# Optimization experiments

Measured on AMD Instinct MI355X. Metric: run time of the kernel, lower is better.

Reference implementation:

```python
import jax, jax.numpy as jnp
import numpy as np

NEG_SLOPE = 0.2

def _gat_conv(x, src, dst, W, a_src, a_dst, b, heads, out_ch, concat):
    N = x.shape[0]
    h = (x @ W).reshape(N, heads, out_ch)                      # [N,H,C]
    al_s = jnp.einsum('nhc,hc->nh', h, a_src)                  # [N,H]
    al_d = jnp.einsum('nhc,hc->nh', h, a_dst)
    e = jax.nn.leaky_relu(al_s[src] + al_d[dst], NEG_SLOPE)    # [E,H]
    emax = jax.ops.segment_max(e, dst, num_segments=N)         # [N,H]
    ex = jnp.exp(e - emax[dst])
    denom = jax.ops.segment_sum(ex, dst, num_segments=N)
    alpha = ex / denom[dst]                                    # [E,H]
    msg = h[src] * alpha[:, :, None]                           # [E,H,C]
    out = jax.ops.segment_sum(msg, dst, num_segments=N)        # [N,H,C]
    if concat:
        out = out.reshape(N, heads * out_ch)
    else:
        out = out.mean(axis=1)
    return out + b

def _add_self_loops(edge_index, N):
    loops = jnp.arange(N, dtype=edge_index.dtype)
    src = jnp.concatenate([edge_index[0], loops])
    dst = jnp.concatenate([edge_index[1], loops])
    return src, dst

def setup_inputs() -> dict:
    key = jax.random.key(0)
    ks = jax.random.split(key, 16)
    N, E, Fin, C, H, G, OUT = 50000, 1600000, 128, 32, 8, 256, 64
    s = 0.05
    inp = {
        'x': jax.random.normal(ks[0], (N, Fin), jnp.float32),
        'edge_index': jax.random.randint(ks[1], (2, E), 0, N, jnp.int64),
        'batch': jnp.sort(jax.random.randint(ks[2], (N,), 0, G, jnp.int64)),
        'W0': jax.random.normal(ks[3], (Fin, H * C), jnp.float32) * s,
        'a_src0': jax.random.normal(ks[4], (H, C), jnp.float32) * s,
        'a_dst0': jax.random.normal(ks[5], (H, C), jnp.float32) * s,
        'b0': jnp.zeros((H * C,), jnp.float32),
        'W1': jax.random.normal(ks[6], (H * C, H * C), jnp.float32) * s,
        'a_src1': jax.random.normal(ks[7], (H, C), jnp.float32) * s,
        'a_dst1': jax.random.normal(ks[8], (H, C), jnp.float32) * s,
        'b1': jnp.zeros((H * C,), jnp.float32),
        'W2': jax.random.normal(ks[9], (H * C, C), jnp.float32) * s,
        'a_src2': jax.random.normal(ks[10], (1, C), jnp.float32) * s,
        'a_dst2': jax.random.normal(ks[11], (1, C), jnp.float32) * s,
        'b2': jnp.zeros((C,), jnp.float32),
        'lin_w': jax.random.normal(ks[12], (C, OUT), jnp.float32) * s,
        'lin_b': jnp.zeros((OUT,), jnp.float32),
    }
    return inp

def reference(x, edge_index, batch, W0, a_src0, a_dst0, b0, W1, a_src1, a_dst1, b1,
              W2, a_src2, a_dst2, b2, lin_w, lin_b):
    N = x.shape[0]
    G = 256
    src, dst = _add_self_loops(edge_index, N)
    h = jax.nn.relu(_gat_conv(x, src, dst, W0, a_src0, a_dst0, b0, 8, 32, True))
    h = jax.nn.relu(_gat_conv(h, src, dst, W1, a_src1, a_dst1, b1, 8, 32, True))
    h = _gat_conv(h, src, dst, W2, a_src2, a_dst2, b2, 1, 32, True)  # heads=1 concat -> [N,32]
    # global mean pool over graphs
    sums = jax.ops.segment_sum(h, batch, num_segments=G)
    cnts = jax.ops.segment_sum(jnp.ones((N,), h.dtype), batch, num_segments=G)
    pooled = sums / jnp.maximum(cnts, 1.0)[:, None]
    return pooled @ lin_w + lin_b
```

## Files before the change

### kernel.cpp

```cpp
#include <hip/hip_runtime.h>
#include <hip/hip_bf16.h>


#define LRELU(x) ((x) >= 0.f ? (x) : 0.2f * (x))

typedef unsigned short ushort8 __attribute__((ext_vector_type(8)));
typedef unsigned short ushort4v __attribute__((ext_vector_type(4)));
typedef __attribute__((ext_vector_type(8))) short bf16x8;
typedef __attribute__((ext_vector_type(4))) float f32x4;
typedef __attribute__((ext_vector_type(2))) float f32x2;

__device__ __forceinline__ float bf2f(unsigned short u) {
    return __uint_as_float(((unsigned)u) << 16);
}
__device__ __forceinline__ unsigned short f2bf(float f) {
    __hip_bfloat16 b = __float2bfloat16(f);
    return *reinterpret_cast<unsigned short*>(&b);
}
__device__ __forceinline__ void gl_lds16(const unsigned short* g, unsigned short* l) {
    __builtin_amdgcn_global_load_lds((const __attribute__((address_space(1))) void*)g,
                                     (__attribute__((address_space(3))) void*)l, 16, 0, 0);
}


__global__ void deg_kernel(const int* __restrict__ dst, int* __restrict__ deg,
                           int E, int N) {
    int i = blockIdx.x * blockDim.x + threadIdx.x;
    if (i < E) atomicAdd(&deg[dst[i]], 1);
    else if (i < E + N) atomicAdd(&deg[i - E], 1);
}

__global__ void scan_kernel(const int* __restrict__ deg, int* __restrict__ rowptr,
                            int n) {
    __shared__ int partial[1024];
    const int tid = threadIdx.x;
    const int chunk = (n + 1023) / 1024;
    const int start = min(tid * chunk, n);
    const int end = min(start + chunk, n);
    int s = 0;
    for (int i = start; i < end; i++) s += deg[i];
    partial[tid] = s;
    __syncthreads();
    for (int o = 1; o < 1024; o <<= 1) {
        int v = (tid >= o) ? partial[tid - o] : 0;
        __syncthreads();
        partial[tid] += v;
        __syncthreads();
    }
    int run = (tid == 0) ? 0 : partial[tid - 1];
    for (int i = start; i < end; i++) { rowptr[i] = run; run += deg[i]; }
    if (tid == 0) rowptr[n] = partial[1023];
}

__global__ void scatter_col_binned(const int* __restrict__ src, const int* __restrict__ dst,
                                   int* __restrict__ rowptr, int* __restrict__ col,
                                   int E, int N, int lo, int hi) {
    int i = blockIdx.x * blockDim.x + threadIdx.x;
    if (i < E) {
        int d = dst[i];
        if (d < lo || d >= hi) return;
        int pos = atomicAdd(&rowptr[d], 1);
        col[pos] = src[i];
    } else if (i < E + N) {
        int d = i - E;
        if (d < lo || d >= hi) return;
        int pos = atomicAdd(&rowptr[d], 1);
        col[pos] = d;
    }
}

__global__ void expand_dst_kernel(const int* __restrict__ rowptr, int* __restrict__ dstA,
                                  int N) {
    int n = blockIdx.x * blockDim.x + threadIdx.x;
    if (n >= N) return;
    int r0 = (n == 0) ? 0 : rowptr[n - 1];
    int r1 = rowptr[n];
    for (int p = r0; p < r1; p++) dstA[p] = n;
}

__global__ void gstart_kernel(const int* __restrict__ batch, int* __restrict__ gstart,
                              int N, int G) {
    int g = blockIdx.x * blockDim.x + threadIdx.x;
    if (g > G) return;
    int lo = 0, hi = N;
    while (lo < hi) { int mid = (lo + hi) >> 1; if (batch[mid] < g) lo = mid + 1; else hi = mid; }
    gstart[g] = lo;
}


__global__ void split_plain_kernel(const float* __restrict__ X, unsigned short* __restrict__ h,
                                   unsigned short* __restrict__ l, int n) {
    int i = blockIdx.x * blockDim.x + threadIdx.x;
    if (i >= n) return;
    float v = X[i];
    unsigned short hb = f2bf(v);
    h[i] = hb;
    l[i] = f2bf(v - bf2f(hb));
}

__global__ void splitT_kernel(const float* __restrict__ W, unsigned short* __restrict__ th,
                              unsigned short* __restrict__ tl, int K, int N) {
    int i = blockIdx.x * blockDim.x + threadIdx.x;
    if (i >= N * K) return;
    int n = i / K, k = i - n * K;
    float v = W[(size_t)k * N + n];
    unsigned short hb = f2bf(v);
    th[i] = hb;
    tl[i] = f2bf(v - bf2f(hb));
}


template <int BM, int BN, int WM, int WN>
__global__ __launch_bounds__(256)
void gemm_mfma_v2(const unsigned short* __restrict__ Ah, const unsigned short* __restrict__ Al,
                  const unsigned short* __restrict__ Bth, const unsigned short* __restrict__ Btl,
                  unsigned short* __restrict__ Cc, int M, int N, int K) {
    constexpr int BK = 32;
    constexpr int MT = WM / 16, NT = WN / 16;
    constexpr int NWX = BN / WN;
    __shared__ __attribute__((aligned(16))) unsigned short Ha[BM][BK];
    __shared__ __attribute__((aligned(16))) unsigned short La[BM][BK];
    __shared__ __attribute__((aligned(16))) unsigned short Hb[BN][BK];
    __shared__ __attribute__((aligned(16))) unsigned short Lb[BN][BK];
    const int tid = threadIdx.x;
    const int lane = tid & 63;
    const int wave = tid >> 6;
    const int wx = wave % NWX, wy = wave / NWX;
    const int by = blockIdx.y * BM;
    const int bx = blockIdx.x * BN;
    const int r16 = lane & 15, kg = lane >> 4;
    const int srow = lane >> 2, sslot = lane & 3;

    f32x4 acc[MT][NT];
#pragma unroll
    for (int i = 0; i < MT; i++)
#pragma unroll
        for (int j = 0; j < NT; j++) acc[i][j] = (f32x4){0.f, 0.f, 0.f, 0.f};

    for (int k0 = 0; k0 < K; k0 += BK) {
        for (int t = wave; t < BM / 16; t += 4) {
            int gm = by + t * 16 + srow;
            if (gm >= M) gm = M - 1;
            const size_t goff = (size_t)gm * K + k0 + sslot * 8;
            gl_lds16(Ah + goff, &Ha[t * 16][0]);
            gl_lds16(Al + goff, &La[t * 16][0]);
        }
        for (int t = wave; t < BN / 16; t += 4) {
            int gn = bx + t * 16 + srow;
            const size_t goff = (size_t)gn * K + k0 + sslot * 8;
            gl_lds16(Bth + goff, &Hb[t * 16][0]);
            gl_lds16(Btl + goff, &Lb[t * 16][0]);
        }
        __syncthreads();
        bf16x8 bh[NT], bl[NT];
#pragma unroll
        for (int j = 0; j < NT; j++) {
            bh[j] = *(const bf16x8*)&Hb[wx * WN + j * 16 + r16][kg * 8];
            bl[j] = *(const bf16x8*)&Lb[wx * WN + j * 16 + r16][kg * 8];
        }
#pragma unroll
        for (int i = 0; i < MT; i++) {
            bf16x8 ah = *(const bf16x8*)&Ha[wy * WM + i * 16 + r16][kg * 8];
            bf16x8 al2 = *(const bf16x8*)&La[wy * WM + i * 16 + r16][kg * 8];
#pragma unroll
            for (int j = 0; j < NT; j++) {
                acc[i][j] = __builtin_amdgcn_mfma_f32_16x16x32_bf16(ah, bh[j], acc[i][j], 0, 0, 0);
                acc[i][j] = __builtin_amdgcn_mfma_f32_16x16x32_bf16(ah, bl[j], acc[i][j], 0, 0, 0);
                acc[i][j] = __builtin_amdgcn_mfma_f32_16x16x32_bf16(al2, bh[j], acc[i][j], 0, 0, 0);
            }
        }
        __syncthreads();
    }
#pragma unroll
    for (int i = 0; i < MT; i++) {
#pragma unroll
        for (int r = 0; r < 4; r++) {
            int gm = by + wy * WM + i * 16 + kg * 4 + r;
            if (gm >= M) continue;
#pragma unroll
            for (int j = 0; j < NT; j++) {
                int gn = bx + wx * WN + j * 16 + r16;
                Cc[(size_t)gm * N + gn] = f2bf(acc[i][j][r]);
            }
        }
    }
}


template <int H, int C>
__global__ void al_bf16(const unsigned short* __restrict__ hfeat, const float* __restrict__ a_src,
                        const float* __restrict__ a_dst, float* __restrict__ als,
                        float* __restrict__ ald, int N) {
    int i = blockIdx.x * blockDim.x + threadIdx.x;
    if (i >= N * H) return;
    int n = i / H, h = i % H;
    const unsigned short* hp = hfeat + (size_t)n * H * C + h * C;
    float s1 = 0.f, s2 = 0.f;
    for (int c0 = 0; c0 < C; c0 += 8) {
        ushort8 v = *(const ushort8*)(hp + c0);
#pragma unroll
        for (int k = 0; k < 8; k++) {
            float f = bf2f(v[k]);
            s1 += f * a_src[h * C + c0 + k];
            s2 += f * a_dst[h * C + c0 + k];
        }
    }
    als[i] = s1;
    ald[i] = s2;
}


__global__ void edge_w_pair(const float* __restrict__ als, const float* __restrict__ ald,
                            const int* __restrict__ col, const int* __restrict__ dstA,
                            unsigned int* __restrict__ wts2, int Etot) {
    int i = blockIdx.x * blockDim.x + threadIdx.x;
    if (i >= Etot * 4) return;
    int pos = i >> 2, hp = i & 3;
    int s = col[pos], d = dstA[pos];
    float2 a = *(const float2*)&als[(size_t)s * 8 + hp * 2];
    float2 b = *(const float2*)&ald[(size_t)d * 8 + hp * 2];
    float e0 = a.x + b.x; e0 = LRELU(e0);
    float e1 = a.y + b.y; e1 = LRELU(e1);
    unsigned lo = f2bf(__expf(e0));
    unsigned hi = f2bf(__expf(e1));
    wts2[i] = lo | (hi << 16);
}

__global__ void edge_w_h1(const float* __restrict__ als, const float* __restrict__ ald,
                          const int* __restrict__ col, const int* __restrict__ dstA,
                          unsigned short* __restrict__ wts, int Etot) {
    int i = blockIdx.x * blockDim.x + threadIdx.x;
    if (i >= Etot) return;
    int s = col[i], d = dstA[i];
    float e = als[s] + ald[d];
    e = LRELU(e);
    wts[i] = f2bf(__expf(e));
}


__global__ __launch_bounds__(256)
void gat_agg_w8(const unsigned short* __restrict__ hfeat,
                const unsigned short* __restrict__ wts,
                const int* __restrict__ rowptr,
                const int* __restrict__ col,
                const float* __restrict__ bias,
                unsigned short* __restrict__ outH, unsigned short* __restrict__ outL,
                int N) {
    constexpr int CAP = 128;
    const int wid = threadIdx.x >> 6;
    const int lane = threadIdx.x & 63;
    const int n = blockIdx.x * 4 + wid;
    __shared__ float se_all[4][CAP * 8];
    __shared__ int scol_all[4][CAP];
    if (n >= N) return;
    float* se = se_all[wid];
    int* scol = scol_all[wid];

    const int r0 = (n == 0) ? 0 : rowptr[n - 1];
    const int deg = rowptr[n] - r0;
    const int dh8 = deg * 8;
    const size_t wbase = (size_t)r0 * 8;
    const int dcap = min(deg, CAP);

    for (int j = lane; j < dcap; j += 64) scol[j] = col[r0 + j];

    float p0 = 0.f, p1 = 0.f, p2 = 0.f, p3 = 0.f, p4 = 0.f, p5 = 0.f, p6 = 0.f, p7 = 0.f;
    for (int base = 0; base < dh8; base += 512) {
        int idx = base + lane * 8;
        if (idx < dh8) {
            ushort8 v = *(const ushort8*)&wts[wbase + idx];
            float f0 = bf2f(v[0]), f1 = bf2f(v[1]), f2 = bf2f(v[2]), f3 = bf2f(v[3]);
            float f4 = bf2f(v[4]), f5 = bf2f(v[5]), f6 = bf2f(v[6]), f7 = bf2f(v[7]);
            p0 += f0; p1 += f1; p2 += f2; p3 += f3;
            p4 += f4; p5 += f5; p6 += f6; p7 += f7;
            if (idx < CAP * 8) {
                *(float4*)&se[idx] = (float4){f0, f1, f2, f3};
                *(float4*)&se[idx + 4] = (float4){f4, f5, f6, f7};
            }
        }
    }
#pragma unroll
    for (int m = 1; m < 64; m <<= 1) {
        p0 += __shfl_xor(p0, m); p1 += __shfl_xor(p1, m);
        p2 += __shfl_xor(p2, m); p3 += __shfl_xor(p3, m);
        p4 += __shfl_xor(p4, m); p5 += __shfl_xor(p5, m);
        p6 += __shfl_xor(p6, m); p7 += __shfl_xor(p7, m);
    }
    const int q = lane >> 3;
    float S = (q == 0) ? p0 : (q == 1) ? p1 : (q == 2) ? p2 : (q == 3) ? p3
            : (q == 4) ? p4 : (q == 5) ? p5 : (q == 6) ? p6 : p7;
    const float sinv = 1.0f / S;

    const int cb = lane * 4;
    f32x2 acc01 = {0.f, 0.f}, acc23 = {0.f, 0.f};
    int j = 0;
    for (; j + 7 < dcap; j += 8) {
        int s[8];
#pragma unroll
        for (int u = 0; u < 8; u++) s[u] = __builtin_amdgcn_readfirstlane(scol[j + u]);
        uint2 d[8];
#pragma unroll
        for (int u = 0; u < 8; u++) d[u] = *(const uint2*)(hfeat + (size_t)s[u] * 256 + cb);
#pragma unroll
        for (int u = 0; u < 8; u++) {
            float w = se[(j + u) * 8 + q];
            f32x2 wp = {w, w};
            acc01 += (f32x2){__uint_as_float(d[u].x << 16),
                             __uint_as_float(d[u].x & 0xffff0000u)} * wp;
            acc23 += (f32x2){__uint_as_float(d[u].y << 16),
                             __uint_as_float(d[u].y & 0xffff0000u)} * wp;
        }
    }
    for (; j < dcap; j++) {
        int s0 = __builtin_amdgcn_readfirstlane(scol[j]);
        uint2 d = *(const uint2*)(hfeat + (size_t)s0 * 256 + cb);
        float w = se[j * 8 + q];
        f32x2 wp = {w, w};
        acc01 += (f32x2){__uint_as_float(d.x << 16), __uint_as_float(d.x & 0xffff0000u)} * wp;
        acc23 += (f32x2){__uint_as_float(d.y << 16), __uint_as_float(d.y & 0xffff0000u)} * wp;
    }
    for (; j < deg; j++) {
        int s0 = col[r0 + j];
        float w = bf2f(wts[wbase + (size_t)j * 8 + q]);
        uint2 d = *(const uint2*)(hfeat + (size_t)s0 * 256 + cb);
        f32x2 wp = {w, w};
        acc01 += (f32x2){__uint_as_float(d.x << 16), __uint_as_float(d.x & 0xffff0000u)} * wp;
        acc23 += (f32x2){__uint_as_float(d.y << 16), __uint_as_float(d.y & 0xffff0000u)} * wp;
    }

    float4 b4 = *(const float4*)&bias[cb];
    float o0 = fmaxf(acc01.x * sinv + b4.x, 0.f);
    float o1 = fmaxf(acc01.y * sinv + b4.y, 0.f);
    float o2 = fmaxf(acc23.x * sinv + b4.z, 0.f);
    float o3 = fmaxf(acc23.y * sinv + b4.w, 0.f);
    unsigned short h0 = f2bf(o0), h1 = f2bf(o1), h2 = f2bf(o2), h3 = f2bf(o3);
    const size_t ob = (size_t)n * 256 + cb;
    *(ushort4v*)&outH[ob] = (ushort4v){h0, h1, h2, h3};
    *(ushort4v*)&outL[ob] = (ushort4v){f2bf(o0 - bf2f(h0)), f2bf(o1 - bf2f(h1)),
                                       f2bf(o2 - bf2f(h2)), f2bf(o3 - bf2f(h3))};
}


__global__ __launch_bounds__(256)
void gat_agg_h1w(const unsigned short* __restrict__ hfeat,
                 const unsigned short* __restrict__ wts,
                 const int* __restrict__ rowptr, const int* __restrict__ col,
                 const float* __restrict__ bias, float* __restrict__ out, int N) {
    constexpr int CAP = 256;
    const int wid = threadIdx.x >> 6;
    const int lane = threadIdx.x & 63;
    const int n = blockIdx.x * 4 + wid;
    __shared__ float sw_all[4][CAP];
    __shared__ int scol_all[4][CAP];
    if (n >= N) return;
    float* sw = sw_all[wid];
    int* scol = scol_all[wid];

    const int r0 = (n == 0) ? 0 : rowptr[n - 1];
    const int deg = rowptr[n] - r0;
    const int dcap = min(deg, CAP);

    float lsum = 0.f;
    for (int idx = lane; idx < deg; idx += 64) {
        float v = bf2f(wts[r0 + idx]);
        if (idx < CAP) { sw[idx] = v; scol[idx] = col[r0 + idx]; }
        lsum += v;
    }
#pragma unroll
    for (int m = 1; m < 64; m <<= 1) lsum += __shfl_xor(lsum, m);
    const float sinv = 1.0f / lsum;

    const int slot = lane >> 3, ch = lane & 7;
    f32x2 acc01 = {0.f, 0.f}, acc23 = {0.f, 0.f};
    for (int j = 0; j < dcap; j += 8) {
        int e = j + slot;
        int ec = min(e, dcap - 1);
        int s = scol[ec];
        float w = (e < dcap) ? sw[ec] : 0.f;
        uint2 d = *(const uint2*)(hfeat + (size_t)s * 32 + ch * 4);
        f32x2 wp = {w, w};
        acc01 += (f32x2){__uint_as_float(d.x << 16), __uint_as_float(d.x & 0xffff0000u)} * wp;
        acc23 += (f32x2){__uint_as_float(d.y << 16), __uint_as_float(d.y & 0xffff0000u)} * wp;
    }
    for (int j = CAP; j < deg; j += 8) {
        int e = j + slot;
        int ec = min(e, deg - 1);
        int s = col[r0 + ec];
        float w = (e < deg) ? bf2f(wts[r0 + ec]) : 0.f;
        uint2 d = *(const uint2*)(hfeat + (size_t)s * 32 + ch * 4);
        f32x2 wp = {w, w};
        acc01 += (f32x2){__uint_as_float(d.x << 16), __uint_as_float(d.x & 0xffff0000u)} * wp;
        acc23 += (f32x2){__uint_as_float(d.y << 16), __uint_as_float(d.y & 0xffff0000u)} * wp;
    }
#pragma unroll
    for (int m = 8; m < 64; m <<= 1) {
        acc01.x += __shfl_xor(acc01.x, m);
        acc01.y += __shfl_xor(acc01.y, m);
        acc23.x += __shfl_xor(acc23.x, m);
        acc23.y += __shfl_xor(acc23.y, m);
    }
    if (slot == 0) {
        float4 b4 = *(const float4*)&bias[ch * 4];
        float4 o;
        o.x = acc01.x * sinv + b4.x;
        o.y = acc01.y * sinv + b4.y;
        o.z = acc23.x * sinv + b4.z;
        o.w = acc23.y * sinv + b4.w;
        *(float4*)&out[(size_t)n * 32 + ch * 4] = o;
    }
}


__global__ __launch_bounds__(256)
void pool_final_kernel(const float* __restrict__ h, const int* __restrict__ gstart,
                       const float* __restrict__ lin_w, const float* __restrict__ lin_b,
                       float* __restrict__ out) {
    const int g = blockIdx.x;
    const int tid = threadIdx.x;
    const int n0 = gstart[g], n1 = gstart[g + 1];
    const int r = tid >> 5, c = tid & 31;
    __shared__ float pp[4][32];
    __shared__ float pm[32];
    float acc = 0.f;
    for (int n = n0 + r; n < n1; n += 8) acc += h[(size_t)n * 32 + c];
    acc += __shfl_xor(acc, 32);
    if ((tid & 63) < 32) pp[tid >> 6][c] = acc;
    __syncthreads();
    if (tid < 32) {
        float s = pp[0][tid] + pp[1][tid] + pp[2][tid] + pp[3][tid];
        pm[tid] = s / fmaxf((float)(n1 - n0), 1.f);
    }
    __syncthreads();
    if (tid < 64) {
        float a = lin_b[tid];
#pragma unroll 8
        for (int cc = 0; cc < 32; cc++) a += pm[cc] * lin_w[cc * 64 + tid];
        out[(size_t)g * 64 + tid] = a;
    }
}


extern "C" void kernel_launch(void* const* d_in, const int* in_sizes, int n_in,
                              void* d_out, int out_size, void* d_ws, size_t ws_size,
                              hipStream_t stream) {
    const float* x     = (const float*)d_in[0];
    const int*   ei    = (const int*)d_in[1];
    const int*   batch = (const int*)d_in[2];
    const float* W0    = (const float*)d_in[3];
    const float* a_s0  = (const float*)d_in[4];
    const float* a_d0  = (const float*)d_in[5];
    const float* b0    = (const float*)d_in[6];
    const float* W1    = (const float*)d_in[7];
    const float* a_s1  = (const float*)d_in[8];
    const float* a_d1  = (const float*)d_in[9];
    const float* b1    = (const float*)d_in[10];
    const float* W2    = (const float*)d_in[11];
    const float* a_s2  = (const float*)d_in[12];
    const float* a_d2  = (const float*)d_in[13];
    const float* b2    = (const float*)d_in[14];
    const float* lin_w = (const float*)d_in[15];
    const float* lin_b = (const float*)d_in[16];

    const int N = in_sizes[0] / 128;
    const int E = in_sizes[1] / 2;
    const int G = 256;
    const int Etot = E + N;
    const int* src = ei;
    const int* dst = ei + E;

    char* w = (char*)d_ws;
    size_t off = 0;
    auto alloc = [&](size_t bytes) -> void* {
        void* p = (void*)(w + off);
        off += (bytes + 255) & ~(size_t)255;
        return p;
    };
    int* deg    = (int*)alloc((size_t)N * 4);
    int* rowptr = (int*)alloc((size_t)(N + 1) * 4);
    int* colA   = (int*)alloc((size_t)Etot * 4);
    int* dstA   = (int*)alloc((size_t)Etot * 4);
    int* gstart = (int*)alloc((size_t)(G + 1) * 4);
    float* als  = (float*)alloc((size_t)N * 8 * 4);
    float* ald  = (float*)alloc((size_t)N * 8 * 4);
    unsigned short* hb  = (unsigned short*)alloc((size_t)N * 256 * 2);
    unsigned short* wts = (unsigned short*)alloc((size_t)Etot * 8 * 2);
    unsigned short* g0h = (unsigned short*)alloc((size_t)N * 256 * 2);
    unsigned short* g0l = (unsigned short*)alloc((size_t)N * 256 * 2);
    float* out2 = (float*)alloc((size_t)N * 32 * 4);
    unsigned short* w0h = (unsigned short*)alloc((size_t)128 * 256 * 2);
    unsigned short* w0l = (unsigned short*)alloc((size_t)128 * 256 * 2);
    unsigned short* w1h = (unsigned short*)alloc((size_t)256 * 256 * 2);
    unsigned short* w1l = (unsigned short*)alloc((size_t)256 * 256 * 2);
    unsigned short* w2h = (unsigned short*)alloc((size_t)256 * 32 * 2);
    unsigned short* w2l = (unsigned short*)alloc((size_t)256 * 32 * 2);
    unsigned short* xh = g0h;
    unsigned short* xl = g0h + (size_t)N * 128;

    hipMemsetAsync(deg, 0, (size_t)N * 4, stream);

    deg_kernel<<<(Etot + 255) / 256, 256, 0, stream>>>(dst, deg, E, N);
    scan_kernel<<<1, 1024, 0, stream>>>(deg, rowptr, N);
    for (int p = 0; p < 2; p++) {
        int lo = (int)((size_t)N * p / 2);
        int hi = (int)((size_t)N * (p + 1) / 2);
        scatter_col_binned<<<(Etot + 255) / 256, 256, 0, stream>>>(src, dst, rowptr, colA, E, N, lo, hi);
    }
    expand_dst_kernel<<<(N + 255) / 256, 256, 0, stream>>>(rowptr, dstA, N);
    gstart_kernel<<<2, 256, 0, stream>>>(batch, gstart, N, G);

    split_plain_kernel<<<(N * 128 + 255) / 256, 256, 0, stream>>>(x, xh, xl, N * 128);
    splitT_kernel<<<(128 * 256 + 255) / 256, 256, 0, stream>>>(W0, w0h, w0l, 128, 256);
    splitT_kernel<<<(256 * 256 + 255) / 256, 256, 0, stream>>>(W1, w1h, w1l, 256, 256);
    splitT_kernel<<<(256 * 32 + 255) / 256, 256, 0, stream>>>(W2, w2h, w2l, 256, 32);

    const int MB = (N + 127) / 128;

    gemm_mfma_v2<128, 128, 64, 64><<<dim3(2, MB), 256, 0, stream>>>(xh, xl, w0h, w0l, hb, N, 256, 128);
    al_bf16<8, 32><<<(N * 8 + 255) / 256, 256, 0, stream>>>(hb, a_s0, a_d0, als, ald, N);
    edge_w_pair<<<((size_t)Etot * 4 + 255) / 256, 256, 0, stream>>>(als, ald, colA, dstA, (unsigned int*)wts, Etot);
    gat_agg_w8<<<(N + 3) / 4, 256, 0, stream>>>(hb, wts, rowptr, colA, b0, g0h, g0l, N);

    gemm_mfma_v2<128, 128, 64, 64><<<dim3(2, MB), 256, 0, stream>>>(g0h, g0l, w1h, w1l, hb, N, 256, 256);
    al_bf16<8, 32><<<(N * 8 + 255) / 256, 256, 0, stream>>>(hb, a_s1, a_d1, als, ald, N);
    edge_w_pair<<<((size_t)Etot * 4 + 255) / 256, 256, 0, stream>>>(als, ald, colA, dstA, (unsigned int*)wts, Etot);
    gat_agg_w8<<<(N + 3) / 4, 256, 0, stream>>>(hb, wts, rowptr, colA, b1, g0h, g0l, N);

    gemm_mfma_v2<128, 32, 32, 32><<<dim3(1, MB), 256, 0, stream>>>(g0h, g0l, w2h, w2l, hb, N, 32, 256);
    al_bf16<1, 32><<<(N + 255) / 256, 256, 0, stream>>>(hb, a_s2, a_d2, als, ald, N);
    edge_w_h1<<<(Etot + 255) / 256, 256, 0, stream>>>(als, ald, colA, dstA, wts, Etot);
    gat_agg_h1w<<<(N + 3) / 4, 256, 0, stream>>>(hb, wts, rowptr, colA, b2, out2, N);

    pool_final_kernel<<<G, 256, 0, stream>>>(out2, gstart, lin_w, lin_b, (float*)d_out);
}
```

Measured before the change: 685.5 us.

## Sort CSR neighbor lists by source-node bucket to improve gather locality

Builds a per-destination 16-bucket histogram keyed by source-node range and scatters column indices into bucket slots, so each node's neighbor list is roughly sorted by source id. The aim is better L2/cache locality when the aggregation kernels gather source features. The rowptr convention changes to exclusive starts. The aggregation inner loops are also rewritten from packed f32x2 math with 8-way unroll to scalar FMAs with 4-way unroll. This adds extra preprocessing kernels, a larger atomic histogram and more memory traffic.

```diff
diff --git a/kernel.cpp b/kernel.cpp
--- a/kernel.cpp
+++ b/kernel.cpp
@@ -8,7 +8,6 @@
 typedef unsigned short ushort4v __attribute__((ext_vector_type(4)));
 typedef __attribute__((ext_vector_type(8))) short bf16x8;
 typedef __attribute__((ext_vector_type(4))) float f32x4;
-typedef __attribute__((ext_vector_type(2))) float f32x2;
 
 __device__ __forceinline__ float bf2f(unsigned short u) {
     return __uint_as_float(((unsigned)u) << 16);
@@ -22,12 +21,27 @@
                                      (__attribute__((address_space(3))) void*)l, 16, 0, 0);
 }
 
-
-__global__ void deg_kernel(const int* __restrict__ dst, int* __restrict__ deg,
-                           int E, int N) {
-    int i = blockIdx.x * blockDim.x + threadIdx.x;
-    if (i < E) atomicAdd(&deg[dst[i]], 1);
-    else if (i < E + N) atomicAdd(&deg[i - E], 1);
+#define NBUCK 16
+
+
+__global__ void hist16_kernel(const int* __restrict__ src, const int* __restrict__ dst,
+                              int* __restrict__ bcnt, int E, int N) {
+    int i = blockIdx.x * blockDim.x + threadIdx.x;
+    int s, d;
+    if (i < E) { s = src[i]; d = dst[i]; }
+    else if (i < E + N) { s = i - E; d = s; }
+    else return;
+    int b = (s * NBUCK) / N;
+    atomicAdd(&bcnt[d * NBUCK + b], 1);
+}
+
+__global__ void node_deg_kernel(const int* __restrict__ bcnt, int* __restrict__ deg, int N) {
+    int n = blockIdx.x * blockDim.x + threadIdx.x;
+    if (n >= N) return;
+    int s = 0;
+#pragma unroll
+    for (int b = 0; b < NBUCK; b++) s += bcnt[n * NBUCK + b];
+    deg[n] = s;
 }
 
 __global__ void scan_kernel(const int* __restrict__ deg, int* __restrict__ rowptr,
@@ -52,29 +66,43 @@
     if (tid == 0) rowptr[n] = partial[1023];
 }
 
+__global__ void bstart_fill_kernel(const int* __restrict__ bcnt, const int* __restrict__ rowptr,
+                                   int* __restrict__ bstart, int N) {
+    int n = blockIdx.x * blockDim.x + threadIdx.x;
+    if (n >= N) return;
+    int base = rowptr[n];
+#pragma unroll
+    for (int b = 0; b < NBUCK; b++) {
+        bstart[n * NBUCK + b] = base;
+        base += bcnt[n * NBUCK + b];
+    }
+}
+
 __global__ void scatter_col_binned(const int* __restrict__ src, const int* __restrict__ dst,
-                                   int* __restrict__ rowptr, int* __restrict__ col,
+                                   int* __restrict__ bstart, int* __restrict__ col,
                                    int E, int N, int lo, int hi) {
     int i = blockIdx.x * blockDim.x + threadIdx.x;
+    int s, d;
     if (i < E) {
-        int d = dst[i];
+        d = dst[i];
         if (d < lo || d >= hi) return;
-        int pos = atomicAdd(&rowptr[d], 1);
-        col[pos] = src[i];
+        s = src[i];
     } else if (i < E + N) {
-        int d = i - E;
+        d = i - E;
         if (d < lo || d >= hi) return;
-        int pos = atomicAdd(&rowptr[d], 1);
-        col[pos] = d;
-    }
+        s = d;
+    } else return;
+    int b = (s * NBUCK) / N;
+    int pos = atomicAdd(&bstart[d * NBUCK + b], 1);
+    col[pos] = s;
 }
 
 __global__ void expand_dst_kernel(const int* __restrict__ rowptr, int* __restrict__ dstA,
                                   int N) {
     int n = blockIdx.x * blockDim.x + threadIdx.x;
     if (n >= N) return;
-    int r0 = (n == 0) ? 0 : rowptr[n - 1];
-    int r1 = rowptr[n];
+    int r0 = rowptr[n];
+    int r1 = rowptr[n + 1];
     for (int p = r0; p < r1; p++) dstA[p] = n;
 }
 
@@ -256,8 +284,8 @@
     float* se = se_all[wid];
     int* scol = scol_all[wid];
 
-    const int r0 = (n == 0) ? 0 : rowptr[n - 1];
-    const int deg = rowptr[n] - r0;
+    const int r0 = rowptr[n];
+    const int deg = rowptr[n + 1] - r0;
     const int dh8 = deg * 8;
     const size_t wbase = (size_t)r0 * 8;
     const int dcap = min(deg, CAP);
@@ -292,47 +320,44 @@
     const float sinv = 1.0f / S;
 
     const int cb = lane * 4;
-    f32x2 acc01 = {0.f, 0.f}, acc23 = {0.f, 0.f};
+    float a0 = 0.f, a1 = 0.f, a2 = 0.f, a3 = 0.f;
     int j = 0;
-    for (; j + 7 < dcap; j += 8) {
-        int s[8];
-#pragma unroll
-        for (int u = 0; u < 8; u++) s[u] = __builtin_amdgcn_readfirstlane(scol[j + u]);
-        uint2 d[8];
-#pragma unroll
-        for (int u = 0; u < 8; u++) d[u] = *(const uint2*)(hfeat + (size_t)s[u] * 256 + cb);
-#pragma unroll
-        for (int u = 0; u < 8; u++) {
-            float w = se[(j + u) * 8 + q];
-            f32x2 wp = {w, w};
-            acc01 += (f32x2){__uint_as_float(d[u].x << 16),
-                             __uint_as_float(d[u].x & 0xffff0000u)} * wp;
-            acc23 += (f32x2){__uint_as_float(d[u].y << 16),
-                             __uint_as_float(d[u].y & 0xffff0000u)} * wp;
-        }
+    for (; j + 3 < dcap; j += 4) {
+        int s0 = __builtin_amdgcn_readfirstlane(scol[j]);
+        int s1 = __builtin_amdgcn_readfirstlane(scol[j + 1]);
+        int s2 = __builtin_amdgcn_readfirstlane(scol[j + 2]);
+        int s3 = __builtin_amdgcn_readfirstlane(scol[j + 3]);
+        ushort4v v0 = *(const ushort4v*)(hfeat + (size_t)s0 * 256 + cb);
+        ushort4v v1 = *(const ushort4v*)(hfeat + (size_t)s1 * 256 + cb);
+        ushort4v v2 = *(const ushort4v*)(hfeat + (size_t)s2 * 256 + cb);
+        ushort4v v3 = *(const ushort4v*)(hfeat + (size_t)s3 * 256 + cb);
+        float w0 = se[j * 8 + q];
+        float w1 = se[j * 8 + 8 + q];
+        float w2 = se[j * 8 + 16 + q];
+        float w3 = se[j * 8 + 24 + q];
+        a0 += bf2f(v0[0]) * w0; a1 += bf2f(v0[1]) * w0; a2 += bf2f(v0[2]) * w0; a3 += bf2f(v0[3]) * w0;
+        a0 += bf2f(v1[0]) * w1; a1 += bf2f(v1[1]) * w1; a2 += bf2f(v1[2]) * w1; a3 += bf2f(v1[3]) * w1;
+        a0 += bf2f(v2[0]) * w2; a1 += bf2f(v2[1]) * w2; a2 += bf2f(v2[2]) * w2; a3 += bf2f(v2[3]) * w2;
+        a0 += bf2f(v3[0]) * w3; a1 += bf2f(v3[1]) * w3; a2 += bf2f(v3[2]) * w3; a3 += bf2f(v3[3]) * w3;
     }
     for (; j < dcap; j++) {
         int s0 = __builtin_amdgcn_readfirstlane(scol[j]);
-        uint2 d = *(const uint2*)(hfeat + (size_t)s0 * 256 + cb);
-        float w = se[j * 8 + q];
-        f32x2 wp = {w, w};
-        acc01 += (f32x2){__uint_as_float(d.x << 16), __uint_as_float(d.x & 0xffff0000u)} * wp;
-        acc23 += (f32x2){__uint_as_float(d.y << 16), __uint_as_float(d.y & 0xffff0000u)} * wp;
+        ushort4v v0 = *(const ushort4v*)(hfeat + (size_t)s0 * 256 + cb);
+        float w0 = se[j * 8 + q];
+        a0 += bf2f(v0[0]) * w0; a1 += bf2f(v0[1]) * w0; a2 += bf2f(v0[2]) * w0; a3 += bf2f(v0[3]) * w0;
     }
     for (; j < deg; j++) {
         int s0 = col[r0 + j];
-        float w = bf2f(wts[wbase + (size_t)j * 8 + q]);
-        uint2 d = *(const uint2*)(hfeat + (size_t)s0 * 256 + cb);
-        f32x2 wp = {w, w};
-        acc01 += (f32x2){__uint_as_float(d.x << 16), __uint_as_float(d.x & 0xffff0000u)} * wp;
-        acc23 += (f32x2){__uint_as_float(d.y << 16), __uint_as_float(d.y & 0xffff0000u)} * wp;
+        float w0 = bf2f(wts[wbase + (size_t)j * 8 + q]);
+        ushort4v v0 = *(const ushort4v*)(hfeat + (size_t)s0 * 256 + cb);
+        a0 += bf2f(v0[0]) * w0; a1 += bf2f(v0[1]) * w0; a2 += bf2f(v0[2]) * w0; a3 += bf2f(v0[3]) * w0;
     }
 
     float4 b4 = *(const float4*)&bias[cb];
-    float o0 = fmaxf(acc01.x * sinv + b4.x, 0.f);
-    float o1 = fmaxf(acc01.y * sinv + b4.y, 0.f);
-    float o2 = fmaxf(acc23.x * sinv + b4.z, 0.f);
-    float o3 = fmaxf(acc23.y * sinv + b4.w, 0.f);
+    float o0 = fmaxf(a0 * sinv + b4.x, 0.f);
+    float o1 = fmaxf(a1 * sinv + b4.y, 0.f);
+    float o2 = fmaxf(a2 * sinv + b4.z, 0.f);
+    float o3 = fmaxf(a3 * sinv + b4.w, 0.f);
     unsigned short h0 = f2bf(o0), h1 = f2bf(o1), h2 = f2bf(o2), h3 = f2bf(o3);
     const size_t ob = (size_t)n * 256 + cb;
     *(ushort4v*)&outH[ob] = (ushort4v){h0, h1, h2, h3};
@@ -356,8 +381,8 @@
     float* sw = sw_all[wid];
     int* scol = scol_all[wid];
 
-    const int r0 = (n == 0) ? 0 : rowptr[n - 1];
-    const int deg = rowptr[n] - r0;
+    const int r0 = rowptr[n];
+    const int deg = rowptr[n + 1] - r0;
     const int dcap = min(deg, CAP);
 
     float lsum = 0.f;
@@ -371,41 +396,39 @@
     const float sinv = 1.0f / lsum;
 
     const int slot = lane >> 3, ch = lane & 7;
-    f32x2 acc01 = {0.f, 0.f}, acc23 = {0.f, 0.f};
+    float a0 = 0.f, a1 = 0.f, a2 = 0.f, a3 = 0.f;
     for (int j = 0; j < dcap; j += 8) {
         int e = j + slot;
         int ec = min(e, dcap - 1);
         int s = scol[ec];
         float w = (e < dcap) ? sw[ec] : 0.f;
-        uint2 d = *(const uint2*)(hfeat + (size_t)s * 32 + ch * 4);
-        f32x2 wp = {w, w};
-        acc01 += (f32x2){__uint_as_float(d.x << 16), __uint_as_float(d.x & 0xffff0000u)} * wp;
-        acc23 += (f32x2){__uint_as_float(d.y << 16), __uint_as_float(d.y & 0xffff0000u)} * wp;
+        ushort4v v = *(const ushort4v*)(hfeat + (size_t)s * 32 + ch * 4);
+        a0 += bf2f(v[0]) * w; a1 += bf2f(v[1]) * w;
+        a2 += bf2f(v[2]) * w; a3 += bf2f(v[3]) * w;
     }
     for (int j = CAP; j < deg; j += 8) {
         int e = j + slot;
         int ec = min(e, deg - 1);
         int s = col[r0 + ec];
         float w = (e < deg) ? bf2f(wts[r0 + ec]) : 0.f;
-        uint2 d = *(const uint2*)(hfeat + (size_t)s * 32 + ch * 4);
-        f32x2 wp = {w, w};
-        acc01 += (f32x2){__uint_as_float(d.x << 16), __uint_as_float(d.x & 0xffff0000u)} * wp;
-        acc23 += (f32x2){__uint_as_float(d.y << 16), __uint_as_float(d.y & 0xffff0000u)} * wp;
+        ushort4v v = *(const ushort4v*)(hfeat + (size_t)s * 32 + ch * 4);
+        a0 += bf2f(v[0]) * w; a1 += bf2f(v[1]) * w;
+        a2 += bf2f(v[2]) * w; a3 += bf2f(v[3]) * w;
     }
 #pragma unroll
     for (int m = 8; m < 64; m <<= 1) {
-        acc01.x += __shfl_xor(acc01.x, m);
-        acc01.y += __shfl_xor(acc01.y, m);
-        acc23.x += __shfl_xor(acc23.x, m);
-        acc23.y += __shfl_xor(acc23.y, m);
+        a0 += __shfl_xor(a0, m);
+        a1 += __shfl_xor(a1, m);
+        a2 += __shfl_xor(a2, m);
+        a3 += __shfl_xor(a3, m);
     }
     if (slot == 0) {
         float4 b4 = *(const float4*)&bias[ch * 4];
         float4 o;
-        o.x = acc01.x * sinv + b4.x;
-        o.y = acc01.y * sinv + b4.y;
-        o.z = acc23.x * sinv + b4.z;
-        o.w = acc23.y * sinv + b4.w;
+        o.x = a0 * sinv + b4.x;
+        o.y = a1 * sinv + b4.y;
+        o.z = a2 * sinv + b4.z;
+        o.w = a3 * sinv + b4.w;
         *(float4*)&out[(size_t)n * 32 + ch * 4] = o;
     }
 }
@@ -475,6 +498,8 @@
         off += (bytes + 255) & ~(size_t)255;
         return p;
     };
+    int* bcnt   = (int*)alloc((size_t)N * NBUCK * 4);
+    int* bstart = (int*)alloc((size_t)N * NBUCK * 4);
     int* deg    = (int*)alloc((size_t)N * 4);
     int* rowptr = (int*)alloc((size_t)(N + 1) * 4);
     int* colA   = (int*)alloc((size_t)Etot * 4);
@@ -496,14 +521,16 @@
     unsigned short* xh = g0h;
     unsigned short* xl = g0h + (size_t)N * 128;
 
-    hipMemsetAsync(deg, 0, (size_t)N * 4, stream);
-
-    deg_kernel<<<(Etot + 255) / 256, 256, 0, stream>>>(dst, deg, E, N);
+    hipMemsetAsync(bcnt, 0, (size_t)N * NBUCK * 4, stream);
+
+    hist16_kernel<<<(Etot + 255) / 256, 256, 0, stream>>>(src, dst, bcnt, E, N);
+    node_deg_kernel<<<(N + 255) / 256, 256, 0, stream>>>(bcnt, deg, N);
     scan_kernel<<<1, 1024, 0, stream>>>(deg, rowptr, N);
+    bstart_fill_kernel<<<(N + 255) / 256, 256, 0, stream>>>(bcnt, rowptr, bstart, N);
     for (int p = 0; p < 2; p++) {
         int lo = (int)((size_t)N * p / 2);
         int hi = (int)((size_t)N * (p + 1) / 2);
-        scatter_col_binned<<<(Etot + 255) / 256, 256, 0, stream>>>(src, dst, rowptr, colA, E, N, lo, hi);
+        scatter_col_binned<<<(Etot + 255) / 256, 256, 0, stream>>>(src, dst, bstart, colA, E, N, lo, hi);
     }
     expand_dst_kernel<<<(N + 255) / 256, 256, 0, stream>>>(rowptr, dstA, N);
     gstart_kernel<<<2, 256, 0, stream>>>(batch, gstart, N, G);
```

After: 693.7 us. About the same (+1.2%).
